# Performance work log

Measured on AMD Instinct MI355X. Metric: run time of the kernel, lower is better.

Reference implementation:

```python
import jax, jax.numpy as jnp
import numpy as np

B, T, D_HID, D_TRK, N_TRANS = 128, 40, 512, 256, 64


def setup_inputs() -> dict:
    key = jax.random.key(0)
    ks = jax.random.split(key, 8)
    d, t = D_HID, D_TRK
    s = 0.05
    return {
        "buffers": jax.random.normal(ks[0], (B, T, 2 * d), jnp.float32),
        "W_left": jax.random.normal(ks[1], (5 * d, d), jnp.float32) * s,
        "b_left": jnp.zeros((5 * d,), jnp.float32),
        "W_right": jax.random.normal(ks[2], (5 * d, d), jnp.float32) * s,
        "W_track": jax.random.normal(ks[3], (5 * d, t), jnp.float32) * s,
        "W_ih": jax.random.normal(ks[4], (4 * t, 3 * d), jnp.float32) * s,
        "W_hh": jax.random.normal(ks[5], (4 * t, t), jnp.float32) * s,
        "b_ih": jnp.zeros((4 * t,), jnp.float32),
        "b_hh": jnp.zeros((4 * t,), jnp.float32),
        "W_trans": jax.random.normal(ks[6], (4, t), jnp.float32) * s,
        "b_trans": jnp.zeros((4,), jnp.float32),
        "transitions": jax.random.randint(ks[7], (N_TRANS, B), 0, 4),
    }


def _spinn_forward(buffers, W_left, b_left, W_right, W_track,
                   W_ih, W_hh, b_ih, b_hh, W_trans, b_trans, n_steps):
    # Thin-stack style vectorized SPINN: fixed-capacity stack + pointers.
    Bb, Tt, two_d = buffers.shape
    d = two_d // 2
    t = W_hh.shape[1]
    cap = Tt + 2  # stack never exceeds 2 initial + (T-2) shifts
    dtype = buffers.dtype

    stack0 = jnp.zeros((Bb, cap, two_d), dtype)
    # stacks = [buf[0], buf[0]] in the torch code
    stack0 = stack0.at[:, 0].set(buffers[:, 0]).at[:, 1].set(buffers[:, 0])
    sptr0 = jnp.full((Bb,), 2, jnp.int32)   # stack length
    blen0 = jnp.full((Bb,), Tt, jnp.int32)  # buffer length (pops from the end)
    th0 = jnp.zeros((Bb, t), dtype)
    tc0 = jnp.zeros((Bb, t), dtype)
    bidx = jnp.arange(Bb)

    def step(carry, _):
        stack, sptr, blen, th, tc = carry
        buf_top = buffers[bidx, blen - 1]          # buf[-1], [B, 2d]
        s1 = stack[bidx, sptr - 1]                 # stack[-1]
        s2 = stack[bidx, sptr - 2]                 # stack[-2]
        # Tracker LSTMCell on cat(buf_h, stack1_h, stack2_h)
        x = jnp.concatenate([buf_top[:, :d], s1[:, :d], s2[:, :d]], axis=1)
        gates = x @ W_ih.T + b_ih + th @ W_hh.T + b_hh
        gi, gf, gg, go = jnp.split(gates, 4, axis=1)
        tc_new = jax.nn.sigmoid(gf) * tc + jax.nn.sigmoid(gi) * jnp.tanh(gg)
        th_new = jax.nn.sigmoid(go) * jnp.tanh(tc_new)
        logits = th_new @ W_trans.T + b_trans      # [B, 4]
        trans = jnp.argmax(logits, axis=1)
        do_shift = (trans == 3) & (blen > 2)
        do_red = (trans == 2) & (sptr > 3)
        # REDUCE (TreeLSTM) computed for all rows, masked in below.
        # left = stack[-2], right = stack[-1] (right popped first in torch).
        lstm_in = (s2[:, :d] @ W_left.T + b_left
                   + s1[:, :d] @ W_right.T
                   + th_new @ W_track.T)           # [B, 5d]
        a, i_, f1, f2, o_ = jnp.split(lstm_in, 5, axis=1)
        c = (jnp.tanh(a) * jax.nn.sigmoid(i_)
             + jax.nn.sigmoid(f1) * s2[:, d:]
             + jax.nn.sigmoid(f2) * s1[:, d:])
        h = jax.nn.sigmoid(o_) * jnp.tanh(c)
        node = jnp.concatenate([h, c], axis=1)
        # SHIFT: push buf_top; REDUCE: overwrite stack[-2] and shrink by 1.
        stack = stack.at[bidx, sptr].set(
            jnp.where(do_shift[:, None], buf_top, stack[bidx, sptr]))
        stack = stack.at[bidx, sptr - 2].set(
            jnp.where(do_red[:, None], node, stack[bidx, sptr - 2]))
        sptr = sptr + do_shift.astype(jnp.int32) - do_red.astype(jnp.int32)
        blen = blen - do_shift.astype(jnp.int32)
        return (stack, sptr, blen, th_new, tc_new), logits

    _, all_logits = jax.lax.scan(step, (stack0, sptr0, blen0, th0, tc0),
                                 None, length=n_steps)
    return all_logits  # [n_steps, B, 4] = stacked trans_preds_batch


def reference(buffers, W_left, b_left, W_right, W_track, W_ih, W_hh,
              b_ih, b_hh, W_trans, b_trans, transitions):
    n_steps = transitions.shape[0]  # torch only uses transitions.size(0)
    return _spinn_forward(buffers, W_left, b_left, W_right, W_track,
                          W_ih, W_hh, b_ih, b_hh, W_trans, b_trans, n_steps)
```

## Files before the change

### kernel.cpp

```cpp
#include <hip/hip_runtime.h>
#include <math.h>


#define B_ 128
#define CAP 42
#define XW 2048
#define GSPLIT 14
#define LSPLIT 8

__device__ __forceinline__ float sigm(float x) { return 1.f / (1.f + expf(-x)); }

__global__ void k_repack(const float* __restrict__ W_ih, const float* __restrict__ W_hh,
                         const float* __restrict__ W_left, const float* __restrict__ W_right,
                         const float* __restrict__ W_track, const float* __restrict__ b_ih,
                         const float* __restrict__ b_hh,
                         float* __restrict__ W1T, float* __restrict__ W2T,
                         float* __restrict__ W3T, float* __restrict__ b1) {
    size_t idx = (size_t)blockIdx.x * 256 + threadIdx.x;
    const size_t n1 = 1792ull * 1024ull;
    const size_t n2 = 1024ull * 2560ull;
    const size_t n3 = 256ull * 2560ull;
    if (idx < n1) {
        int k = (int)(idx >> 10), n = (int)(idx & 1023);
        W1T[idx] = (k < 1536) ? W_ih[(size_t)n * 1536 + k] : W_hh[(size_t)n * 256 + (k - 1536)];
    } else if (idx < n1 + n2) {
        size_t r = idx - n1;
        int k = (int)(r / 2560), n = (int)(r % 2560);
        W2T[r] = (k < 512) ? W_right[(size_t)n * 512 + k] : W_left[(size_t)n * 512 + (k - 512)];
    } else if (idx < n1 + n2 + n3) {
        size_t r = idx - n1 - n2;
        int k = (int)(r / 2560), n = (int)(r % 2560);
        W3T[r] = W_track[(size_t)n * 256 + k];
    } else if (idx < n1 + n2 + n3 + 1024) {
        int i = (int)(idx - n1 - n2 - n3);
        b1[i] = b_ih[i] + b_hh[i];
    }
}

__global__ void k_init(const float* __restrict__ buffers, float* __restrict__ stack,
                       float* __restrict__ X, float* __restrict__ tc,
                       int* __restrict__ sptr, int* __restrict__ blen) {
    int b = blockIdx.x, t = threadIdx.x;
    const float* b0 = buffers + (size_t)b * 40 * 1024;
    const float* btop = b0 + 39 * 1024;
    float* stk = stack + (size_t)b * CAP * 1024;
    for (int j = t; j < 1024; j += 256) { stk[j] = b0[j]; stk[1024 + j] = b0[j]; }
    float* Xb = X + (size_t)b * XW;
    for (int j = t; j < 512; j += 256) {
        Xb[j] = btop[j]; Xb[512 + j] = b0[j]; Xb[1024 + j] = b0[j];
    }
    Xb[1536 + t] = 0.f;
    tc[b * 256 + t] = 0.f;
    if (t == 0) { sptr[b] = 2; blen[b] = 40; }
}

__global__ __launch_bounds__(256, 3) void k_gemm(const float* __restrict__ X,
                                                 const float* __restrict__ W1T,
                                                 const float* __restrict__ W2T,
                                                 float* __restrict__ gpart,
                                                 float* __restrict__ lpart) {
    __shared__ float As[32][132];
    __shared__ float Ws[32][68];
    const int bid = blockIdx.x;
    const float* WT; float* out; int N, n0, k0, aoff;
    if (bid < 224) {
        int ks = bid >> 4, nb = bid & 15;
        WT = W1T; out = gpart + (size_t)ks * 128 * 1024;
        N = 1024; n0 = nb * 64; k0 = ks * 128; aoff = 0;
    } else {
        int b2 = bid - 224; int ks = b2 / 40, nb = b2 % 40;
        WT = W2T; out = lpart + (size_t)ks * 128 * 2560;
        N = 2560; n0 = nb * 64; k0 = ks * 128; aoff = 512;
    }
    const int tid = threadIdx.x;
    const int tm = tid >> 4;
    const int tn = tid & 15;

    float acc[8][4];
#pragma unroll
    for (int i = 0; i < 8; i++)
#pragma unroll
        for (int j = 0; j < 4; j++) acc[i][j] = 0.f;

    for (int ki = 0; ki < 128; ki += 32) {
        const int kb = k0 + ki;
        __syncthreads();
        {
            int m = tid >> 1;
            int c8 = (tid & 1) * 16;
            const float4* src = (const float4*)(X + (size_t)m * XW + aoff + kb + c8);
#pragma unroll
            for (int j = 0; j < 4; j++) {
                float4 v = src[j];
                int kk = c8 + j * 4;
                As[kk + 0][m] = v.x; As[kk + 1][m] = v.y; As[kk + 2][m] = v.z; As[kk + 3][m] = v.w;
            }
        }
        {
            int kk = tid >> 3;
            int c = (tid & 7) * 8;
            const float4* src = (const float4*)(WT + (size_t)(kb + kk) * N + n0 + c);
            float4* dst = (float4*)(&Ws[kk][c]);
            dst[0] = src[0]; dst[1] = src[1];
        }
        __syncthreads();
#pragma unroll 4
        for (int kk = 0; kk < 32; kk++) {
            float a[8], w[4];
            *(float4*)&a[0] = *(const float4*)&As[kk][tm * 4];
            *(float4*)&a[4] = *(const float4*)&As[kk][64 + tm * 4];
            *(float4*)&w[0] = *(const float4*)&Ws[kk][tn * 4];
#pragma unroll
            for (int i = 0; i < 8; i++)
#pragma unroll
                for (int j = 0; j < 4; j++) acc[i][j] += a[i] * w[j];
        }
    }
    float* base = out + n0 + tn * 4;
#pragma unroll
    for (int i = 0; i < 8; i++) {
        int m = (i < 4) ? (tm * 4 + i) : (64 + tm * 4 + (i - 4));
        *(float4*)(base + (size_t)m * N) = make_float4(acc[i][0], acc[i][1], acc[i][2], acc[i][3]);
    }
}

__global__ __launch_bounds__(256) void k_B(const float* __restrict__ gpart,
                                           const float* __restrict__ lpart,
                                           const float* __restrict__ b1,
                                           const float* __restrict__ b_left,
                                           const float* __restrict__ W3T,
                                           const float* __restrict__ W_trans,
                                           const float* __restrict__ b_trans,
                                           const float* __restrict__ buffers,
                                           float* __restrict__ stack,
                                           float* __restrict__ X,
                                           const float* __restrict__ tc_in,
                                           float* __restrict__ tc_out,
                                           const int* __restrict__ sp_in,
                                           int* __restrict__ sp_out,
                                           const int* __restrict__ bl_in,
                                           int* __restrict__ bl_out,
                                           float* __restrict__ out_s) {
    const int bid = blockIdx.x;
    const int b = bid >> 2, q = bid & 3;
    const int t = threadIdx.x;
    const int sp = sp_in[b], bl = bl_in[b];

    const float* gp = gpart + (size_t)b * 1024;
    float gi = b1[t], gf = b1[256 + t], gg = b1[512 + t], go = b1[768 + t];
#pragma unroll
    for (int kc = 0; kc < GSPLIT; kc++) {
        const float* p = gp + (size_t)kc * 128 * 1024;
        gi += p[t]; gf += p[256 + t]; gg += p[512 + t]; go += p[768 + t];
    }
    float tcv = tc_in[b * 256 + t];
    float tcn = sigm(gf) * tcv + sigm(gi) * tanhf(gg);
    float thn = sigm(go) * tanhf(tcn);

    __shared__ float sh_th[256];
    __shared__ float red[256][4];
    sh_th[t] = thn;
    red[t][0] = thn * W_trans[t];
    red[t][1] = thn * W_trans[256 + t];
    red[t][2] = thn * W_trans[512 + t];
    red[t][3] = thn * W_trans[768 + t];
    __syncthreads();
    for (int off = 128; off > 0; off >>= 1) {
        if (t < off) {
            red[t][0] += red[t + off][0]; red[t][1] += red[t + off][1];
            red[t][2] += red[t + off][2]; red[t][3] += red[t + off][3];
        }
        __syncthreads();
    }
    float lg[4]; int tr = 0; float best = -1e30f;
#pragma unroll
    for (int l = 0; l < 4; l++) {
        lg[l] = red[0][l] + b_trans[l];
        if (lg[l] > best) { best = lg[l]; tr = l; }
    }
    if (q == 0 && t == 0) {
#pragma unroll
        for (int l = 0; l < 4; l++) out_s[b * 4 + l] = lg[l];
    }
    const bool do_shift = (tr == 3) && (bl > 2);
    const bool do_red   = (tr == 2) && (sp > 3);
    const int spn = sp + (do_shift ? 1 : 0) - (do_red ? 1 : 0);
    const int bln = bl - (do_shift ? 1 : 0);
    float* stk = stack + (size_t)b * CAP * 1024;

    float node_h = 0.f;
    if (do_red && t < 128) {
        const int j = q * 128 + t;
        const float* lp = lpart + (size_t)b * 2560;
        float a  = b_left[j],        ii = b_left[512 + j], f1 = b_left[1024 + j],
              f2 = b_left[1536 + j], oo = b_left[2048 + j];
#pragma unroll
        for (int kc = 0; kc < LSPLIT; kc++) {
            const float* p = lp + (size_t)kc * 128 * 2560;
            a += p[j]; ii += p[512 + j]; f1 += p[1024 + j]; f2 += p[1536 + j]; oo += p[2048 + j];
        }
        const float* w = W3T + j;
#pragma unroll 4
        for (int k = 0; k < 256; k++) {
            float th = sh_th[k];
            const float* wk = w + (size_t)k * 2560;
            a += th * wk[0]; ii += th * wk[512]; f1 += th * wk[1024];
            f2 += th * wk[1536]; oo += th * wk[2048];
        }
        float s1c = stk[(size_t)(sp - 1) * 1024 + 512 + j];
        float s2c = stk[(size_t)(sp - 2) * 1024 + 512 + j];
        float c = tanhf(a) * sigm(ii) + sigm(f1) * s2c + sigm(f2) * s1c;
        float h = sigm(oo) * tanhf(c);
        stk[(size_t)(sp - 2) * 1024 + j] = h;
        stk[(size_t)(sp - 2) * 1024 + 512 + j] = c;
        node_h = h;
    }
    if (do_shift) {
        const float* bt = buffers + ((size_t)b * 40 + (bl - 1)) * 1024;
        const int idx = q * 256 + t;
        stk[(size_t)sp * 1024 + idx] = bt[idx];
    }
    float* Xb = X + (size_t)b * XW;
    if (t < 128) {
        const int j = q * 128 + t;
        const float* btn = buffers + ((size_t)b * 40 + (bln - 1)) * 1024;
        Xb[j] = btn[j];
        float s1h;
        if (do_red)        s1h = node_h;
        else if (do_shift) s1h = buffers[((size_t)b * 40 + (bl - 1)) * 1024 + j];
        else               s1h = stk[(size_t)(sp - 1) * 1024 + j];
        Xb[512 + j] = s1h;
        Xb[1024 + j] = stk[(size_t)(spn - 2) * 1024 + j];
    }
    if ((t >> 6) == q) {
        Xb[1536 + t] = thn;
        tc_out[b * 256 + t] = tcn;
    }
    if (q == 0 && t == 0) { sp_out[b] = spn; bl_out[b] = bln; }
}

extern "C" void kernel_launch(void* const* d_in, const int* in_sizes, int n_in,
                              void* d_out, int out_size, void* d_ws, size_t ws_size,
                              hipStream_t stream) {
    const float* buffers = (const float*)d_in[0];
    const float* W_left  = (const float*)d_in[1];
    const float* b_left  = (const float*)d_in[2];
    const float* W_right = (const float*)d_in[3];
    const float* W_track = (const float*)d_in[4];
    const float* W_ih    = (const float*)d_in[5];
    const float* W_hh    = (const float*)d_in[6];
    const float* b_ih    = (const float*)d_in[7];
    const float* b_hh    = (const float*)d_in[8];
    const float* W_trans = (const float*)d_in[9];
    const float* b_trans = (const float*)d_in[10];
    float* out = (float*)d_out;

    float* ws = (float*)d_ws;
    size_t off = 0;
    float* W1T   = ws + off; off += 1792ull * 1024;
    float* W2T   = ws + off; off += 1024ull * 2560;
    float* W3T   = ws + off; off += 256ull * 2560;
    float* b1    = ws + off; off += 1024;
    float* X     = ws + off; off += (size_t)B_ * XW;
    float* tc_a  = ws + off; off += (size_t)B_ * 256;
    float* tc_b  = ws + off; off += (size_t)B_ * 256;
    float* gpart = ws + off; off += (size_t)GSPLIT * B_ * 1024;
    float* lpart = ws + off; off += (size_t)LSPLIT * B_ * 2560;
    float* stack = ws + off; off += (size_t)B_ * CAP * 1024;
    int* sp_a = (int*)(ws + off); off += 128;
    int* sp_b = (int*)(ws + off); off += 128;
    int* bl_a = (int*)(ws + off); off += 128;
    int* bl_b = (int*)(ws + off); off += 128;

    {
        size_t total = 1792ull * 1024 + 1024ull * 2560 + 256ull * 2560 + 1024;
        int blocks = (int)((total + 255) / 256);
        k_repack<<<blocks, 256, 0, stream>>>(W_ih, W_hh, W_left, W_right, W_track, b_ih, b_hh,
                                             W1T, W2T, W3T, b1);
        k_init<<<B_, 256, 0, stream>>>(buffers, stack, X, tc_a, sp_a, bl_a);
    }

    for (int s = 0; s < 64; s++) {
        k_gemm<<<544, 256, 0, stream>>>(X, W1T, W2T, gpart, lpart);
        const float* tci = (s & 1) ? tc_b : tc_a;  float* tco = (s & 1) ? tc_a : tc_b;
        const int*   spi = (s & 1) ? sp_b : sp_a;  int*   spo = (s & 1) ? sp_a : sp_b;
        const int*   bli = (s & 1) ? bl_b : bl_a;  int*   blo = (s & 1) ? bl_a : bl_b;
        k_B<<<512, 256, 0, stream>>>(gpart, lpart, b1, b_left, W3T, W_trans, b_trans,
                                     buffers, stack, X, tci, tco, spi, spo, bli, blo,
                                     out + (size_t)s * B_ * 4);
    }
    (void)in_sizes; (void)n_in; (void)out_size; (void)ws_size;
}
```

Before: 2.547 ms.

## Fuse per-step GEMM and update kernels into one persistent kernel with grid barriers

Result: slower. 8.624 ms (+238.6%).

```diff
diff --git a/kernel.cpp b/kernel.cpp
--- a/kernel.cpp
+++ b/kernel.cpp
@@ -7,8 +7,21 @@
 #define XW 2048
 #define GSPLIT 14
 #define LSPLIT 8
+#define NBLK 544
+#define NSTEP 64
 
 __device__ __forceinline__ float sigm(float x) { return 1.f / (1.f + expf(-x)); }
+
+__device__ __forceinline__ void gbar(unsigned* cnt, unsigned target) {
+    __syncthreads();
+    if (threadIdx.x == 0) {
+        __hip_atomic_fetch_add(cnt, 1u, __ATOMIC_RELEASE, __HIP_MEMORY_SCOPE_AGENT);
+        while (__hip_atomic_fetch_add(cnt, 0u, __ATOMIC_RELAXED, __HIP_MEMORY_SCOPE_AGENT) < target)
+            __builtin_amdgcn_s_sleep(8);
+        __builtin_amdgcn_fence(__ATOMIC_ACQUIRE, "agent");
+    }
+    __syncthreads();
+}
 
 __global__ void k_repack(const float* __restrict__ W_ih, const float* __restrict__ W_hh,
                          const float* __restrict__ W_left, const float* __restrict__ W_right,
@@ -39,7 +52,8 @@
 
 __global__ void k_init(const float* __restrict__ buffers, float* __restrict__ stack,
                        float* __restrict__ X, float* __restrict__ tc,
-                       int* __restrict__ sptr, int* __restrict__ blen) {
+                       int* __restrict__ sptr, int* __restrict__ blen,
+                       unsigned* __restrict__ cnt) {
     int b = blockIdx.x, t = threadIdx.x;
     const float* b0 = buffers + (size_t)b * 40 * 1024;
     const float* btop = b0 + 39 * 1024;
@@ -52,191 +66,210 @@
     Xb[1536 + t] = 0.f;
     tc[b * 256 + t] = 0.f;
     if (t == 0) { sptr[b] = 2; blen[b] = 40; }
-}
-
-__global__ __launch_bounds__(256, 3) void k_gemm(const float* __restrict__ X,
-                                                 const float* __restrict__ W1T,
-                                                 const float* __restrict__ W2T,
-                                                 float* __restrict__ gpart,
-                                                 float* __restrict__ lpart) {
-    __shared__ float As[32][132];
-    __shared__ float Ws[32][68];
+    if (b == 0 && t == 0) *cnt = 0u;
+}
+
+__global__ __launch_bounds__(256, 3) void k_spinn(
+        float* __restrict__ X,
+        const float* __restrict__ W1T, const float* __restrict__ W2T,
+        const float* __restrict__ W3T,
+        float* __restrict__ gpart, float* __restrict__ lpart,
+        const float* __restrict__ b1, const float* __restrict__ b_left,
+        const float* __restrict__ W_trans, const float* __restrict__ b_trans,
+        const float* __restrict__ buffers, float* __restrict__ stack,
+        float* __restrict__ tc_a, float* __restrict__ tc_b,
+        int* __restrict__ sp_a, int* __restrict__ sp_b,
+        int* __restrict__ bl_a, int* __restrict__ bl_b,
+        float* __restrict__ out, unsigned* cnt) {
     const int bid = blockIdx.x;
-    const float* WT; float* out; int N, n0, k0, aoff;
+    const int tid = threadIdx.x;
+
+    const float* WT; float* outp; int N, n0, k0, aoff;
     if (bid < 224) {
         int ks = bid >> 4, nb = bid & 15;
-        WT = W1T; out = gpart + (size_t)ks * 128 * 1024;
+        WT = W1T; outp = gpart + (size_t)ks * 128 * 1024;
         N = 1024; n0 = nb * 64; k0 = ks * 128; aoff = 0;
     } else {
         int b2 = bid - 224; int ks = b2 / 40, nb = b2 % 40;
-        WT = W2T; out = lpart + (size_t)ks * 128 * 2560;
+        WT = W2T; outp = lpart + (size_t)ks * 128 * 2560;
         N = 2560; n0 = nb * 64; k0 = ks * 128; aoff = 512;
     }
-    const int tid = threadIdx.x;
     const int tm = tid >> 4;
     const int tn = tid & 15;
-
-    float acc[8][4];
-#pragma unroll
-    for (int i = 0; i < 8; i++)
-#pragma unroll
-        for (int j = 0; j < 4; j++) acc[i][j] = 0.f;
-
-    for (int ki = 0; ki < 128; ki += 32) {
-        const int kb = k0 + ki;
-        __syncthreads();
-        {
-            int m = tid >> 1;
-            int c8 = (tid & 1) * 16;
-            const float4* src = (const float4*)(X + (size_t)m * XW + aoff + kb + c8);
-#pragma unroll
-            for (int j = 0; j < 4; j++) {
-                float4 v = src[j];
-                int kk = c8 + j * 4;
-                As[kk + 0][m] = v.x; As[kk + 1][m] = v.y; As[kk + 2][m] = v.z; As[kk + 3][m] = v.w;
+    const int brow = bid >> 2, q = bid & 3;
+
+    __shared__ float As[32][132];
+    __shared__ float Ws[32][68];
+    __shared__ float sh_th[256];
+    __shared__ float red[256][4];
+    __shared__ float shg[5][132];
+
+    unsigned epoch = 0;
+    for (int s = 0; s < NSTEP; s++) {
+        float acc[8][4];
+#pragma unroll
+        for (int i = 0; i < 8; i++)
+#pragma unroll
+            for (int j = 0; j < 4; j++) acc[i][j] = 0.f;
+
+        for (int ki = 0; ki < 128; ki += 32) {
+            const int kb = k0 + ki;
+            __syncthreads();
+            {
+                int m = tid >> 1;
+                int c8 = (tid & 1) * 16;
+                const float4* src = (const float4*)(X + (size_t)m * XW + aoff + kb + c8);
+#pragma unroll
+                for (int j = 0; j < 4; j++) {
+                    float4 v = src[j];
+                    int kk = c8 + j * 4;
+                    As[kk + 0][m] = v.x; As[kk + 1][m] = v.y; As[kk + 2][m] = v.z; As[kk + 3][m] = v.w;
+                }
+            }
+            {
+                int kk = tid >> 3;
+                int c = (tid & 7) * 8;
+                const float4* src = (const float4*)(WT + (size_t)(kb + kk) * N + n0 + c);
+                float4* dst = (float4*)(&Ws[kk][c]);
+                dst[0] = src[0]; dst[1] = src[1];
+            }
+            __syncthreads();
+#pragma unroll 4
+            for (int kk = 0; kk < 32; kk++) {
+                float a[8], w[4];
+                *(float4*)&a[0] = *(const float4*)&As[kk][tm * 4];
+                *(float4*)&a[4] = *(const float4*)&As[kk][64 + tm * 4];
+                *(float4*)&w[0] = *(const float4*)&Ws[kk][tn * 4];
+#pragma unroll
+                for (int i = 0; i < 8; i++)
+#pragma unroll
+                    for (int j = 0; j < 4; j++) acc[i][j] += a[i] * w[j];
             }
         }
         {
-            int kk = tid >> 3;
-            int c = (tid & 7) * 8;
-            const float4* src = (const float4*)(WT + (size_t)(kb + kk) * N + n0 + c);
-            float4* dst = (float4*)(&Ws[kk][c]);
-            dst[0] = src[0]; dst[1] = src[1];
+            float* basep = outp + n0 + tn * 4;
+#pragma unroll
+            for (int i = 0; i < 8; i++) {
+                int m = (i < 4) ? (tm * 4 + i) : (64 + tm * 4 + (i - 4));
+                *(float4*)(basep + (size_t)m * N) = make_float4(acc[i][0], acc[i][1], acc[i][2], acc[i][3]);
+            }
         }
-        __syncthreads();
+        epoch++;
+        gbar(cnt, (unsigned)NBLK * epoch);
+
+        if (bid < 512) {
+            const float* tci = (s & 1) ? tc_b : tc_a;  float* tco = (s & 1) ? tc_a : tc_b;
+            const int*   spi = (s & 1) ? sp_b : sp_a;  int*   spo = (s & 1) ? sp_a : sp_b;
+            const int*   bli = (s & 1) ? bl_b : bl_a;  int*   blo = (s & 1) ? bl_a : bl_b;
+            const int b = brow, t = tid;
+            const int sp = spi[b], bl = bli[b];
+
+            const float* gp = gpart + (size_t)b * 1024;
+            float gi = b1[t], gf = b1[256 + t], gg = b1[512 + t], go = b1[768 + t];
+#pragma unroll
+            for (int kc = 0; kc < GSPLIT; kc++) {
+                const float* p = gp + (size_t)kc * 128 * 1024;
+                gi += p[t]; gf += p[256 + t]; gg += p[512 + t]; go += p[768 + t];
+            }
+            float tcv = tci[b * 256 + t];
+            float tcn = sigm(gf) * tcv + sigm(gi) * tanhf(gg);
+            float thn = sigm(go) * tanhf(tcn);
+
+            sh_th[t] = thn;
+            red[t][0] = thn * W_trans[t];
+            red[t][1] = thn * W_trans[256 + t];
+            red[t][2] = thn * W_trans[512 + t];
+            red[t][3] = thn * W_trans[768 + t];
+            __syncthreads();
+            for (int off = 128; off > 0; off >>= 1) {
+                if (t < off) {
+                    red[t][0] += red[t + off][0]; red[t][1] += red[t + off][1];
+                    red[t][2] += red[t + off][2]; red[t][3] += red[t + off][3];
+                }
+                __syncthreads();
+            }
+            float lg[4]; int tr = 0; float best = -1e30f;
+#pragma unroll
+            for (int l = 0; l < 4; l++) {
+                lg[l] = red[0][l] + b_trans[l];
+                if (lg[l] > best) { best = lg[l]; tr = l; }
+            }
+            if (q == 0 && t == 0) {
+                float* os = out + (size_t)s * B_ * 4;
+#pragma unroll
+                for (int l = 0; l < 4; l++) os[b * 4 + l] = lg[l];
+            }
+            const bool do_shift = (tr == 3) && (bl > 2);
+            const bool do_red   = (tr == 2) && (sp > 3);
+            const int spn = sp + (do_shift ? 1 : 0) - (do_red ? 1 : 0);
+            const int bln = bl - (do_shift ? 1 : 0);
+            float* stk = stack + (size_t)b * CAP * 1024;
+
+            float node_h = 0.f;
+            const int jj = t & 127, kh = t >> 7;
+            if (do_red) {
+                const int j = q * 128 + jj;
+                float a, ii, f1, f2, oo;
+                if (kh == 0) {
+                    a  = b_left[j];        ii = b_left[512 + j]; f1 = b_left[1024 + j];
+                    f2 = b_left[1536 + j]; oo = b_left[2048 + j];
+                } else { a = ii = f1 = f2 = oo = 0.f; }
+                const float* lp = lpart + (size_t)b * 2560;
+#pragma unroll
+                for (int kc = kh * 4; kc < kh * 4 + 4; kc++) {
+                    const float* p = lp + (size_t)kc * 128 * 2560;
+                    a += p[j]; ii += p[512 + j]; f1 += p[1024 + j]; f2 += p[1536 + j]; oo += p[2048 + j];
+                }
+                const float* w = W3T + j;
 #pragma unroll 4
-        for (int kk = 0; kk < 32; kk++) {
-            float a[8], w[4];
-            *(float4*)&a[0] = *(const float4*)&As[kk][tm * 4];
-            *(float4*)&a[4] = *(const float4*)&As[kk][64 + tm * 4];
-            *(float4*)&w[0] = *(const float4*)&Ws[kk][tn * 4];
-#pragma unroll
-            for (int i = 0; i < 8; i++)
-#pragma unroll
-                for (int j = 0; j < 4; j++) acc[i][j] += a[i] * w[j];
+                for (int k = kh * 128; k < kh * 128 + 128; k++) {
+                    float th = sh_th[k];
+                    const float* wk = w + (size_t)k * 2560;
+                    a += th * wk[0]; ii += th * wk[512]; f1 += th * wk[1024];
+                    f2 += th * wk[1536]; oo += th * wk[2048];
+                }
+                if (kh == 1) {
+                    shg[0][jj] = a; shg[1][jj] = ii; shg[2][jj] = f1; shg[3][jj] = f2; shg[4][jj] = oo;
+                }
+                __syncthreads();
+                if (kh == 0) {
+                    a += shg[0][jj]; ii += shg[1][jj]; f1 += shg[2][jj];
+                    f2 += shg[3][jj]; oo += shg[4][jj];
+                    float s1c = stk[(size_t)(sp - 1) * 1024 + 512 + j];
+                    float s2c = stk[(size_t)(sp - 2) * 1024 + 512 + j];
+                    float c = tanhf(a) * sigm(ii) + sigm(f1) * s2c + sigm(f2) * s1c;
+                    float h = sigm(oo) * tanhf(c);
+                    stk[(size_t)(sp - 2) * 1024 + j] = h;
+                    stk[(size_t)(sp - 2) * 1024 + 512 + j] = c;
+                    node_h = h;
+                }
+            }
+            if (do_shift) {
+                const float* bt = buffers + ((size_t)b * 40 + (bl - 1)) * 1024;
+                const int idx = q * 256 + t;
+                stk[(size_t)sp * 1024 + idx] = bt[idx];
+            }
+            float* Xb = X + (size_t)b * XW;
+            if (t < 128) {
+                const int j = q * 128 + t;
+                const float* btn = buffers + ((size_t)b * 40 + (bln - 1)) * 1024;
+                Xb[j] = btn[j];
+                float s1h;
+                if (do_red)        s1h = node_h;
+                else if (do_shift) s1h = buffers[((size_t)b * 40 + (bl - 1)) * 1024 + j];
+                else               s1h = stk[(size_t)(sp - 1) * 1024 + j];
+                Xb[512 + j] = s1h;
+                Xb[1024 + j] = stk[(size_t)(spn - 2) * 1024 + j];
+            }
+            if ((t >> 6) == q) {
+                Xb[1536 + t] = thn;
+                tco[b * 256 + t] = tcn;
+            }
+            if (q == 0 && t == 0) { spo[b] = spn; blo[b] = bln; }
         }
-    }
-    float* base = out + n0 + tn * 4;
-#pragma unroll
-    for (int i = 0; i < 8; i++) {
-        int m = (i < 4) ? (tm * 4 + i) : (64 + tm * 4 + (i - 4));
-        *(float4*)(base + (size_t)m * N) = make_float4(acc[i][0], acc[i][1], acc[i][2], acc[i][3]);
-    }
-}
-
-__global__ __launch_bounds__(256) void k_B(const float* __restrict__ gpart,
-                                           const float* __restrict__ lpart,
-                                           const float* __restrict__ b1,
-                                           const float* __restrict__ b_left,
-                                           const float* __restrict__ W3T,
-                                           const float* __restrict__ W_trans,
-                                           const float* __restrict__ b_trans,
-                                           const float* __restrict__ buffers,
-                                           float* __restrict__ stack,
-                                           float* __restrict__ X,
-                                           const float* __restrict__ tc_in,
-                                           float* __restrict__ tc_out,
-                                           const int* __restrict__ sp_in,
-                                           int* __restrict__ sp_out,
-                                           const int* __restrict__ bl_in,
-                                           int* __restrict__ bl_out,
-                                           float* __restrict__ out_s) {
-    const int bid = blockIdx.x;
-    const int b = bid >> 2, q = bid & 3;
-    const int t = threadIdx.x;
-    const int sp = sp_in[b], bl = bl_in[b];
-
-    const float* gp = gpart + (size_t)b * 1024;
-    float gi = b1[t], gf = b1[256 + t], gg = b1[512 + t], go = b1[768 + t];
-#pragma unroll
-    for (int kc = 0; kc < GSPLIT; kc++) {
-        const float* p = gp + (size_t)kc * 128 * 1024;
-        gi += p[t]; gf += p[256 + t]; gg += p[512 + t]; go += p[768 + t];
-    }
-    float tcv = tc_in[b * 256 + t];
-    float tcn = sigm(gf) * tcv + sigm(gi) * tanhf(gg);
-    float thn = sigm(go) * tanhf(tcn);
-
-    __shared__ float sh_th[256];
-    __shared__ float red[256][4];
-    sh_th[t] = thn;
-    red[t][0] = thn * W_trans[t];
-    red[t][1] = thn * W_trans[256 + t];
-    red[t][2] = thn * W_trans[512 + t];
-    red[t][3] = thn * W_trans[768 + t];
-    __syncthreads();
-    for (int off = 128; off > 0; off >>= 1) {
-        if (t < off) {
-            red[t][0] += red[t + off][0]; red[t][1] += red[t + off][1];
-            red[t][2] += red[t + off][2]; red[t][3] += red[t + off][3];
-        }
-        __syncthreads();
-    }
-    float lg[4]; int tr = 0; float best = -1e30f;
-#pragma unroll
-    for (int l = 0; l < 4; l++) {
-        lg[l] = red[0][l] + b_trans[l];
-        if (lg[l] > best) { best = lg[l]; tr = l; }
-    }
-    if (q == 0 && t == 0) {
-#pragma unroll
-        for (int l = 0; l < 4; l++) out_s[b * 4 + l] = lg[l];
-    }
-    const bool do_shift = (tr == 3) && (bl > 2);
-    const bool do_red   = (tr == 2) && (sp > 3);
-    const int spn = sp + (do_shift ? 1 : 0) - (do_red ? 1 : 0);
-    const int bln = bl - (do_shift ? 1 : 0);
-    float* stk = stack + (size_t)b * CAP * 1024;
-
-    float node_h = 0.f;
-    if (do_red && t < 128) {
-        const int j = q * 128 + t;
-        const float* lp = lpart + (size_t)b * 2560;
-        float a  = b_left[j],        ii = b_left[512 + j], f1 = b_left[1024 + j],
-              f2 = b_left[1536 + j], oo = b_left[2048 + j];
-#pragma unroll
-        for (int kc = 0; kc < LSPLIT; kc++) {
-            const float* p = lp + (size_t)kc * 128 * 2560;
-            a += p[j]; ii += p[512 + j]; f1 += p[1024 + j]; f2 += p[1536 + j]; oo += p[2048 + j];
-        }
-        const float* w = W3T + j;
-#pragma unroll 4
-        for (int k = 0; k < 256; k++) {
-            float th = sh_th[k];
-            const float* wk = w + (size_t)k * 2560;
-            a += th * wk[0]; ii += th * wk[512]; f1 += th * wk[1024];
-            f2 += th * wk[1536]; oo += th * wk[2048];
-        }
-        float s1c = stk[(size_t)(sp - 1) * 1024 + 512 + j];
-        float s2c = stk[(size_t)(sp - 2) * 1024 + 512 + j];
-        float c = tanhf(a) * sigm(ii) + sigm(f1) * s2c + sigm(f2) * s1c;
-        float h = sigm(oo) * tanhf(c);
-        stk[(size_t)(sp - 2) * 1024 + j] = h;
-        stk[(size_t)(sp - 2) * 1024 + 512 + j] = c;
-        node_h = h;
-    }
-    if (do_shift) {
-        const float* bt = buffers + ((size_t)b * 40 + (bl - 1)) * 1024;
-        const int idx = q * 256 + t;
-        stk[(size_t)sp * 1024 + idx] = bt[idx];
-    }
-    float* Xb = X + (size_t)b * XW;
-    if (t < 128) {
-        const int j = q * 128 + t;
-        const float* btn = buffers + ((size_t)b * 40 + (bln - 1)) * 1024;
-        Xb[j] = btn[j];
-        float s1h;
-        if (do_red)        s1h = node_h;
-        else if (do_shift) s1h = buffers[((size_t)b * 40 + (bl - 1)) * 1024 + j];
-        else               s1h = stk[(size_t)(sp - 1) * 1024 + j];
-        Xb[512 + j] = s1h;
-        Xb[1024 + j] = stk[(size_t)(spn - 2) * 1024 + j];
-    }
-    if ((t >> 6) == q) {
-        Xb[1536 + t] = thn;
-        tc_out[b * 256 + t] = tcn;
-    }
-    if (q == 0 && t == 0) { sp_out[b] = spn; bl_out[b] = bln; }
+        epoch++;
+        gbar(cnt, (unsigned)NBLK * epoch);
+    }
 }
 
 extern "C" void kernel_launch(void* const* d_in, const int* in_sizes, int n_in,
@@ -271,23 +304,18 @@
     int* sp_b = (int*)(ws + off); off += 128;
     int* bl_a = (int*)(ws + off); off += 128;
     int* bl_b = (int*)(ws + off); off += 128;
+    unsigned* cnt = (unsigned*)(ws + off); off += 64;
 
     {
         size_t total = 1792ull * 1024 + 1024ull * 2560 + 256ull * 2560 + 1024;
         int blocks = (int)((total + 255) / 256);
         k_repack<<<blocks, 256, 0, stream>>>(W_ih, W_hh, W_left, W_right, W_track, b_ih, b_hh,
                                              W1T, W2T, W3T, b1);
-        k_init<<<B_, 256, 0, stream>>>(buffers, stack, X, tc_a, sp_a, bl_a);
-    }
-
-    for (int s = 0; s < 64; s++) {
-        k_gemm<<<544, 256, 0, stream>>>(X, W1T, W2T, gpart, lpart);
-        const float* tci = (s & 1) ? tc_b : tc_a;  float* tco = (s & 1) ? tc_a : tc_b;
-        const int*   spi = (s & 1) ? sp_b : sp_a;  int*   spo = (s & 1) ? sp_a : sp_b;
-        const int*   bli = (s & 1) ? bl_b : bl_a;  int*   blo = (s & 1) ? bl_a : bl_b;
-        k_B<<<512, 256, 0, stream>>>(gpart, lpart, b1, b_left, W3T, W_trans, b_trans,
-                                     buffers, stack, X, tci, tco, spi, spo, bli, blo,
-                                     out + (size_t)s * B_ * 4);
-    }
+        k_init<<<B_, 256, 0, stream>>>(buffers, stack, X, tc_a, sp_a, bl_a, cnt);
+    }
+
+    k_spinn<<<NBLK, 256, 0, stream>>>(X, W1T, W2T, W3T, gpart, lpart, b1, b_left,
+                                      W_trans, b_trans, buffers, stack,
+                                      tc_a, tc_b, sp_a, sp_b, bl_a, bl_b, out, cnt);
     (void)in_sizes; (void)n_in; (void)out_size; (void)ws_size;
 }
```

## Split per-step kernel into tracker kernel and batched tiled tree-node kernel

Applied to the files above, without the earlier changes.

Result: slower. 3.205 ms (+25.9%).

```diff
diff --git a/kernel.cpp b/kernel.cpp
--- a/kernel.cpp
+++ b/kernel.cpp
@@ -7,6 +7,7 @@
 #define XW 2048
 #define GSPLIT 14
 #define LSPLIT 8
+#define NSTEP 64
 
 __device__ __forceinline__ float sigm(float x) { return 1.f / (1.f + expf(-x)); }
 
@@ -124,28 +125,21 @@
     }
 }
 
-__global__ __launch_bounds__(256) void k_B(const float* __restrict__ gpart,
-                                           const float* __restrict__ lpart,
-                                           const float* __restrict__ b1,
-                                           const float* __restrict__ b_left,
-                                           const float* __restrict__ W3T,
-                                           const float* __restrict__ W_trans,
-                                           const float* __restrict__ b_trans,
-                                           const float* __restrict__ buffers,
-                                           float* __restrict__ stack,
-                                           float* __restrict__ X,
-                                           const float* __restrict__ tc_in,
-                                           float* __restrict__ tc_out,
-                                           const int* __restrict__ sp_in,
-                                           int* __restrict__ sp_out,
-                                           const int* __restrict__ bl_in,
-                                           int* __restrict__ bl_out,
-                                           float* __restrict__ out_s) {
-    const int bid = blockIdx.x;
-    const int b = bid >> 2, q = bid & 3;
-    const int t = threadIdx.x;
-    const int sp = sp_in[b], bl = bl_in[b];
-
+__global__ __launch_bounds__(256) void k_mid(const float* __restrict__ gpart,
+                                             const float* __restrict__ b1,
+                                             const float* __restrict__ tc_in,
+                                             float* __restrict__ tc_out,
+                                             float* __restrict__ X,
+                                             float* __restrict__ TH,
+                                             const float* __restrict__ W_trans,
+                                             const float* __restrict__ b_trans,
+                                             const int* __restrict__ sp_in,
+                                             int* __restrict__ sp_out,
+                                             const int* __restrict__ bl_in,
+                                             int* __restrict__ bl_out,
+                                             int* __restrict__ dec,
+                                             float* __restrict__ out_s) {
+    int b = blockIdx.x, t = threadIdx.x;
     const float* gp = gpart + (size_t)b * 1024;
     float gi = b1[t], gf = b1[256 + t], gg = b1[512 + t], go = b1[768 + t];
 #pragma unroll
@@ -156,10 +150,11 @@
     float tcv = tc_in[b * 256 + t];
     float tcn = sigm(gf) * tcv + sigm(gi) * tanhf(gg);
     float thn = sigm(go) * tanhf(tcn);
-
-    __shared__ float sh_th[256];
+    tc_out[b * 256 + t] = tcn;
+    TH[b * 256 + t] = thn;
+    X[(size_t)b * XW + 1536 + t] = thn;
+
     __shared__ float red[256][4];
-    sh_th[t] = thn;
     red[t][0] = thn * W_trans[t];
     red[t][1] = thn * W_trans[256 + t];
     red[t][2] = thn * W_trans[512 + t];
@@ -172,71 +167,141 @@
         }
         __syncthreads();
     }
-    float lg[4]; int tr = 0; float best = -1e30f;
-#pragma unroll
-    for (int l = 0; l < 4; l++) {
-        lg[l] = red[0][l] + b_trans[l];
-        if (lg[l] > best) { best = lg[l]; tr = l; }
-    }
-    if (q == 0 && t == 0) {
-#pragma unroll
-        for (int l = 0; l < 4; l++) out_s[b * 4 + l] = lg[l];
-    }
-    const bool do_shift = (tr == 3) && (bl > 2);
-    const bool do_red   = (tr == 2) && (sp > 3);
-    const int spn = sp + (do_shift ? 1 : 0) - (do_red ? 1 : 0);
-    const int bln = bl - (do_shift ? 1 : 0);
-    float* stk = stack + (size_t)b * CAP * 1024;
-
-    float node_h = 0.f;
-    if (do_red && t < 128) {
-        const int j = q * 128 + t;
-        const float* lp = lpart + (size_t)b * 2560;
-        float a  = b_left[j],        ii = b_left[512 + j], f1 = b_left[1024 + j],
-              f2 = b_left[1536 + j], oo = b_left[2048 + j];
+    if (t == 0) {
+        float lg[4]; int tr = 0; float best = -1e30f;
+#pragma unroll
+        for (int l = 0; l < 4; l++) {
+            lg[l] = red[0][l] + b_trans[l];
+            if (lg[l] > best) { best = lg[l]; tr = l; }
+            out_s[b * 4 + l] = lg[l];
+        }
+        int sp = sp_in[b], bl = bl_in[b];
+        int shv = (tr == 3 && bl > 2) ? 1 : 0;
+        int rdv = (tr == 2 && sp > 3) ? 1 : 0;
+        sp_out[b] = sp + shv - rdv;
+        bl_out[b] = bl - shv;
+        dec[b] = sp | (bl << 6) | (shv << 12) | (rdv << 13);
+    }
+}
+
+__global__ __launch_bounds__(256) void k_node(const float* __restrict__ lpart,
+                                              const float* __restrict__ b_left,
+                                              const float* __restrict__ W3T,
+                                              const float* __restrict__ TH,
+                                              const int* __restrict__ dec,
+                                              const float* __restrict__ buffers,
+                                              float* __restrict__ stack,
+                                              float* __restrict__ X) {
+    const int bid = blockIdx.x;
+    const int jq = bid & 15, rg = bid >> 4;
+    const int j0 = jq * 32, r0 = rg * 16;
+    const int t = threadIdx.x;
+    const int rl = t >> 4, jg = t & 15;
+    const int row = r0 + rl;
+    const int j = j0 + jg * 2;
+
+    __shared__ float th_s[16 * 260];
+    __shared__ float w_s[32 * 160];
+
+    const int d = dec[row];
+    const int sp = d & 63, bl = (d >> 6) & 63;
+    const bool shv = (d >> 12) & 1, rdv = (d >> 13) & 1;
+    const bool anyred = __any(rdv);
+
+#pragma unroll
+    for (int i = 0; i < 4; i++) {
+        int L4 = i * 256 + t;
+        int rr = L4 >> 6, k4 = (L4 & 63) << 2;
+        *(float4*)&th_s[rr * 260 + k4] = *(const float4*)(TH + (size_t)(r0 + rr) * 256 + k4);
+    }
+
+    float2 acc0 = {0,0}, acc1 = {0,0}, acc2 = {0,0}, acc3 = {0,0}, acc4 = {0,0};
+
+    float4 pf[5];
+#pragma unroll
+    for (int i = 0; i < 5; i++) {
+        int L = i * 256 + t, seg = L >> 3, kk = seg / 5, g = seg - kk * 5, off = (L & 7) << 2;
+        pf[i] = *(const float4*)(W3T + (size_t)kk * 2560 + g * 512 + j0 + off);
+    }
+    for (int kc = 0; kc < 8; kc++) {
+#pragma unroll
+        for (int i = 0; i < 5; i++) {
+            int L = i * 256 + t, seg = L >> 3, kk = seg / 5, g = seg - kk * 5, off = (L & 7) << 2;
+            *(float4*)&w_s[kk * 160 + g * 32 + off] = pf[i];
+        }
+        __syncthreads();
+        if (kc < 7) {
+#pragma unroll
+            for (int i = 0; i < 5; i++) {
+                int L = i * 256 + t, seg = L >> 3, kk = seg / 5, g = seg - kk * 5, off = (L & 7) << 2;
+                pf[i] = *(const float4*)(W3T + (size_t)((kc + 1) * 32 + kk) * 2560 + g * 512 + j0 + off);
+            }
+        }
+        if (anyred) {
+            const float* thp = &th_s[rl * 260 + kc * 32];
+            const float* wp = &w_s[jg * 2];
+#pragma unroll 8
+            for (int kk = 0; kk < 32; kk++) {
+                float th = thp[kk];
+                const float* wr = wp + kk * 160;
+                float2 w;
+                w = *(const float2*)(wr);        acc0.x += th * w.x; acc0.y += th * w.y;
+                w = *(const float2*)(wr + 32);   acc1.x += th * w.x; acc1.y += th * w.y;
+                w = *(const float2*)(wr + 64);   acc2.x += th * w.x; acc2.y += th * w.y;
+                w = *(const float2*)(wr + 96);   acc3.x += th * w.x; acc3.y += th * w.y;
+                w = *(const float2*)(wr + 128);  acc4.x += th * w.x; acc4.y += th * w.y;
+            }
+        }
+        __syncthreads();
+    }
+
+    float* stk = stack + (size_t)row * CAP * 1024;
+    float* Xb = X + (size_t)row * XW;
+    const int spn = sp + (shv ? 1 : 0) - (rdv ? 1 : 0);
+    const int bln = bl - (shv ? 1 : 0);
+    const float* bt = buffers + ((size_t)row * 40 + (bl - 1)) * 1024;
+
+    float2 h2;
+    if (rdv) {
+        const float* lp = lpart + (size_t)row * 2560;
+        float2 a  = *(const float2*)(b_left + j);
+        float2 ii = *(const float2*)(b_left + 512 + j);
+        float2 f1 = *(const float2*)(b_left + 1024 + j);
+        float2 f2 = *(const float2*)(b_left + 1536 + j);
+        float2 oo = *(const float2*)(b_left + 2048 + j);
 #pragma unroll
         for (int kc = 0; kc < LSPLIT; kc++) {
             const float* p = lp + (size_t)kc * 128 * 2560;
-            a += p[j]; ii += p[512 + j]; f1 += p[1024 + j]; f2 += p[1536 + j]; oo += p[2048 + j];
-        }
-        const float* w = W3T + j;
-#pragma unroll 4
-        for (int k = 0; k < 256; k++) {
-            float th = sh_th[k];
-            const float* wk = w + (size_t)k * 2560;
-            a += th * wk[0]; ii += th * wk[512]; f1 += th * wk[1024];
-            f2 += th * wk[1536]; oo += th * wk[2048];
-        }
-        float s1c = stk[(size_t)(sp - 1) * 1024 + 512 + j];
-        float s2c = stk[(size_t)(sp - 2) * 1024 + 512 + j];
-        float c = tanhf(a) * sigm(ii) + sigm(f1) * s2c + sigm(f2) * s1c;
-        float h = sigm(oo) * tanhf(c);
-        stk[(size_t)(sp - 2) * 1024 + j] = h;
-        stk[(size_t)(sp - 2) * 1024 + 512 + j] = c;
-        node_h = h;
-    }
-    if (do_shift) {
-        const float* bt = buffers + ((size_t)b * 40 + (bl - 1)) * 1024;
-        const int idx = q * 256 + t;
-        stk[(size_t)sp * 1024 + idx] = bt[idx];
-    }
-    float* Xb = X + (size_t)b * XW;
-    if (t < 128) {
-        const int j = q * 128 + t;
-        const float* btn = buffers + ((size_t)b * 40 + (bln - 1)) * 1024;
-        Xb[j] = btn[j];
-        float s1h;
-        if (do_red)        s1h = node_h;
-        else if (do_shift) s1h = buffers[((size_t)b * 40 + (bl - 1)) * 1024 + j];
-        else               s1h = stk[(size_t)(sp - 1) * 1024 + j];
-        Xb[512 + j] = s1h;
-        Xb[1024 + j] = stk[(size_t)(spn - 2) * 1024 + j];
-    }
-    if ((t >> 6) == q) {
-        Xb[1536 + t] = thn;
-        tc_out[b * 256 + t] = tcn;
-    }
-    if (q == 0 && t == 0) { sp_out[b] = spn; bl_out[b] = bln; }
+            float2 v;
+            v = *(const float2*)(p + j);        a.x += v.x;  a.y += v.y;
+            v = *(const float2*)(p + 512 + j);  ii.x += v.x; ii.y += v.y;
+            v = *(const float2*)(p + 1024 + j); f1.x += v.x; f1.y += v.y;
+            v = *(const float2*)(p + 1536 + j); f2.x += v.x; f2.y += v.y;
+            v = *(const float2*)(p + 2048 + j); oo.x += v.x; oo.y += v.y;
+        }
+        a.x += acc0.x; a.y += acc0.y;  ii.x += acc1.x; ii.y += acc1.y;
+        f1.x += acc2.x; f1.y += acc2.y; f2.x += acc3.x; f2.y += acc3.y;
+        oo.x += acc4.x; oo.y += acc4.y;
+        float2 s1c = *(const float2*)(stk + (size_t)(sp - 1) * 1024 + 512 + j);
+        float2 s2c = *(const float2*)(stk + (size_t)(sp - 2) * 1024 + 512 + j);
+        float cx = tanhf(a.x) * sigm(ii.x) + sigm(f1.x) * s2c.x + sigm(f2.x) * s1c.x;
+        float cy = tanhf(a.y) * sigm(ii.y) + sigm(f1.y) * s2c.y + sigm(f2.y) * s1c.y;
+        h2.x = sigm(oo.x) * tanhf(cx); h2.y = sigm(oo.y) * tanhf(cy);
+        *(float2*)(stk + (size_t)(sp - 2) * 1024 + j) = h2;
+        *(float2*)(stk + (size_t)(sp - 2) * 1024 + 512 + j) = make_float2(cx, cy);
+    } else if (shv) {
+        h2 = *(const float2*)(bt + j);
+    } else {
+        h2 = *(const float2*)(stk + (size_t)(sp - 1) * 1024 + j);
+    }
+    *(float2*)(Xb + 512 + j) = h2;
+    if (shv) {
+        *(float2*)(stk + (size_t)sp * 1024 + j)       = *(const float2*)(bt + j);
+        *(float2*)(stk + (size_t)sp * 1024 + 512 + j) = *(const float2*)(bt + 512 + j);
+    }
+    const float* btn = buffers + ((size_t)row * 40 + (bln - 1)) * 1024;
+    *(float2*)(Xb + j) = *(const float2*)(btn + j);
+    *(float2*)(Xb + 1024 + j) = *(const float2*)(stk + (size_t)(spn - 2) * 1024 + j);
 }
 
 extern "C" void kernel_launch(void* const* d_in, const int* in_sizes, int n_in,
@@ -264,6 +329,7 @@
     float* X     = ws + off; off += (size_t)B_ * XW;
     float* tc_a  = ws + off; off += (size_t)B_ * 256;
     float* tc_b  = ws + off; off += (size_t)B_ * 256;
+    float* TH    = ws + off; off += (size_t)B_ * 256;
     float* gpart = ws + off; off += (size_t)GSPLIT * B_ * 1024;
     float* lpart = ws + off; off += (size_t)LSPLIT * B_ * 2560;
     float* stack = ws + off; off += (size_t)B_ * CAP * 1024;
@@ -271,6 +337,7 @@
     int* sp_b = (int*)(ws + off); off += 128;
     int* bl_a = (int*)(ws + off); off += 128;
     int* bl_b = (int*)(ws + off); off += 128;
+    int* dec  = (int*)(ws + off); off += 128;
 
     {
         size_t total = 1792ull * 1024 + 1024ull * 2560 + 256ull * 2560 + 1024;
@@ -280,14 +347,14 @@
         k_init<<<B_, 256, 0, stream>>>(buffers, stack, X, tc_a, sp_a, bl_a);
     }
 
-    for (int s = 0; s < 64; s++) {
+    for (int s = 0; s < NSTEP; s++) {
         k_gemm<<<544, 256, 0, stream>>>(X, W1T, W2T, gpart, lpart);
         const float* tci = (s & 1) ? tc_b : tc_a;  float* tco = (s & 1) ? tc_a : tc_b;
         const int*   spi = (s & 1) ? sp_b : sp_a;  int*   spo = (s & 1) ? sp_a : sp_b;
         const int*   bli = (s & 1) ? bl_b : bl_a;  int*   blo = (s & 1) ? bl_a : bl_b;
-        k_B<<<512, 256, 0, stream>>>(gpart, lpart, b1, b_left, W3T, W_trans, b_trans,
-                                     buffers, stack, X, tci, tco, spi, spo, bli, blo,
-                                     out + (size_t)s * B_ * 4);
+        k_mid<<<B_, 256, 0, stream>>>(gpart, b1, tci, tco, X, TH, W_trans, b_trans,
+                                      spi, spo, bli, blo, dec, out + (size_t)s * B_ * 4);
+        k_node<<<128, 256, 0, stream>>>(lpart, b_left, W3T, TH, dec, buffers, stack, X);
     }
     (void)in_sizes; (void)n_in; (void)out_size; (void)ws_size;
 }
```
